# Optimization experiments

Hardware: AMD Instinct MI355X
Metric: run time of the kernel (lower is better)

The kernel has to match this reference:

```python
import jax, jax.numpy as jnp
import numpy as np

NEG_INF = -1e9


def setup_inputs() -> dict:
    key = jax.random.key(0)
    k1, k2, k3 = jax.random.split(key, 3)
    B, S, D, N, K = 8, 4096, 1024, 128, 8
    hidden_states = jax.random.normal(k1, (B, S, D), dtype=jnp.float32)
    sentence_indicator = jnp.sort(
        jax.random.randint(k2, (B, S), 0, N), axis=-1).astype(jnp.int64)
    cls_w = jax.random.normal(k3, (D,), dtype=jnp.float32) * (1.0 / np.sqrt(D))
    cls_b = jnp.zeros((), dtype=jnp.float32)
    return {
        "hidden_states": hidden_states,
        "sentence_indicator": sentence_indicator,
        "cls_w": cls_w,
        "cls_b": cls_b,
        "num_sentences": N,
        "extraction_k": K,
    }


def _selection_loop(hidden_states, sentence_indicator, cls_w, cls_b,
                    num_sentences, extraction_k):
    # --- sentence segment-sum pooling (replaces per-sentence masked-sum loop) ---
    seg_sum = jax.vmap(
        lambda h, ind: jax.ops.segment_sum(h, ind, num_segments=num_sentences)
    )(hidden_states, sentence_indicator)               # [B, N, D]
    counts = jax.vmap(
        lambda ind: jax.ops.segment_sum(
            jnp.ones(ind.shape, jnp.float32), ind, num_segments=num_sentences)
    )(sentence_indicator)                              # [B, N]
    sentence_lens = jnp.clip(counts, 1.0)[..., None]   # [B, N, 1], clamp(min=1)
    sentence_mask0 = (counts > 0).astype(jnp.float32)  # valid-sentence mask [B, N]

    B, N, D = seg_sum.shape

    def step(carry, _):
        cur_sum, cur_len, smask, sel = carry
        combined = cur_sum[:, None, :] + seg_sum           # [B, N, D]
        combined_len = cur_len[:, None, :] + sentence_lens  # [B, N, 1]
        pooled = combined / combined_len                    # [B, N, D]
        logits = jnp.einsum('bnd,d->bn', pooled, cls_w) + cls_b
        logits = jnp.where(smask > 0, logits, NEG_INF)      # mask_tensor
        idx = jnp.argmax(logits, axis=-1)                   # eval path (argmax)
        one_hot = jax.nn.one_hot(idx, N, dtype=jnp.float32)  # [B, N]
        smask = (1.0 - one_hot) * smask
        new_sum = jnp.einsum('bn,bnd->bd', one_hot, combined)
        new_len = jnp.sum(one_hot[..., None] * combined_len, axis=1)  # [B, 1]
        return (new_sum, new_len, smask, sel + one_hot), logits

    init = (jnp.zeros((B, D), jnp.float32),
            jnp.zeros((B, 1), jnp.float32),
            sentence_mask0,
            jnp.zeros((B, N), jnp.float32))
    (_, _, _, selected), all_logits = jax.lax.scan(
        step, init, None, length=extraction_k)
    selected = jnp.clip(selected, 0.0, 1.0)  # clamp(max=1)
    return selected, all_logits  # [B,N], [K,B,N]


def reference(hidden_states, sentence_indicator, cls_w, cls_b,
              num_sentences, extraction_k):
    selected_one_hot, all_logits = _selection_loop(
        hidden_states, sentence_indicator, cls_w, cls_b,
        num_sentences, extraction_k)
    # convert_attention_mask: token is kept iff its sentence was selected
    new_attention_mask = jnp.take_along_axis(
        selected_one_hot, sentence_indicator, axis=1)      # [B, S] float 0/1
    masked_hidden_states = new_attention_mask[..., None] * hidden_states
    return selected_one_hot, all_logits, new_attention_mask, masked_hidden_states
```

## Files before the change

kernel.cpp:

```cpp
#include <hip/hip_runtime.h>

#define B_ 8
#define S_ 4096
#define D_ 1024
#define N_ 128
#define K_ 8
#define NEG_INF_ (-1e9f)

__global__ void tok_dot_kernel(const float* __restrict__ h,
                               const float* __restrict__ cls_w,
                               float* __restrict__ tok_dot) {
    const int lane = threadIdx.x & 63;
    const int gw = (blockIdx.x << 2) + (threadIdx.x >> 6);
    const int t0 = gw << 2;
    const int dofs = lane * 4;

    const float4 w0 = *reinterpret_cast<const float4*>(cls_w + 0 * 256 + dofs);
    const float4 w1 = *reinterpret_cast<const float4*>(cls_w + 1 * 256 + dofs);
    const float4 w2 = *reinterpret_cast<const float4*>(cls_w + 2 * 256 + dofs);
    const float4 w3 = *reinterpret_cast<const float4*>(cls_w + 3 * 256 + dofs);

    float acc[4];
    #pragma unroll
    for (int t = 0; t < 4; ++t) {
        const float* p = h + (size_t)(t0 + t) * D_;
        const float4 v0 = *reinterpret_cast<const float4*>(p + 0 * 256 + dofs);
        const float4 v1 = *reinterpret_cast<const float4*>(p + 1 * 256 + dofs);
        const float4 v2 = *reinterpret_cast<const float4*>(p + 2 * 256 + dofs);
        const float4 v3 = *reinterpret_cast<const float4*>(p + 3 * 256 + dofs);
        acc[t] = v0.x * w0.x + v0.y * w0.y + v0.z * w0.z + v0.w * w0.w
               + v1.x * w1.x + v1.y * w1.y + v1.z * w1.z + v1.w * w1.w
               + v2.x * w2.x + v2.y * w2.y + v2.z * w2.z + v2.w * w2.w
               + v3.x * w3.x + v3.y * w3.y + v3.z * w3.z + v3.w * w3.w;
    }
    for (int off = 32; off > 0; off >>= 1) {
        #pragma unroll
        for (int t = 0; t < 4; ++t) acc[t] += __shfl_down(acc[t], off, 64);
    }
    if (lane == 0) {
        *reinterpret_cast<float4*>(tok_dot + t0) =
            make_float4(acc[0], acc[1], acc[2], acc[3]);
    }
}

__global__ void select_kernel(const float* __restrict__ tok_dot,
                              const int* __restrict__ ind,
                              const float* __restrict__ cls_b,
                              float* __restrict__ out_selected,
                              float* __restrict__ out_logits,
                              float* __restrict__ out_mask) {
    const int b = blockIdx.x;
    const int tid = threadIdx.x;

    __shared__ float td[S_];
    __shared__ int   si[S_];
    __shared__ float sh_part[256];
    __shared__ int   sh_s0[N_], sh_s1[N_];
    __shared__ float sh_dseg[N_], sh_len[N_], sh_msk[N_], sh_sel[N_];

    for (int s = tid; s < S_; s += 256) {
        td[s] = tok_dot[b * S_ + s];
        si[s] = ind[b * S_ + s];
    }
    __syncthreads();

    {
        const int n = tid & (N_ - 1);
        int lo = 0, hi = S_;
        while (lo < hi) { int mid = (lo + hi) >> 1; if (si[mid] < n) lo = mid + 1; else hi = mid; }
        const int s0 = lo;
        lo = s0; hi = S_;
        while (lo < hi) { int mid = (lo + hi) >> 1; if (si[mid] < n + 1) lo = mid + 1; else hi = mid; }
        const int s1 = lo;
        const int mid = (s0 + s1) >> 1;
        const int a = (tid < N_) ? s0 : mid;
        const int e = (tid < N_) ? mid : s1;
        float acc = 0.f;
        for (int s = a; s < e; ++s) acc += td[s];
        sh_part[tid] = acc;
        if (tid < N_) { sh_s0[tid] = s0; sh_s1[tid] = s1; }
    }
    __syncthreads();
    if (tid < N_) {
        const int s0 = sh_s0[tid], s1 = sh_s1[tid];
        sh_dseg[tid] = sh_part[tid] + sh_part[tid + N_];
        sh_len[tid]  = fmaxf((float)(s1 - s0), 1.0f);
        sh_msk[tid]  = (s1 > s0) ? 1.f : 0.f;
    }
    __syncthreads();

    if (tid < 64) {
        const float bias = cls_b[0];
        const float d0 = sh_dseg[tid],      d1 = sh_dseg[tid + 64];
        const float l0 = sh_len[tid],       l1 = sh_len[tid + 64];
        float m0 = sh_msk[tid],             m1 = sh_msk[tid + 64];
        float sel0 = 0.f, sel1 = 0.f;
        float dot = 0.f, len = 0.f;

        for (int k = 0; k < K_; ++k) {
            const float lg0 = (m0 > 0.f) ? (dot + d0) / (len + l0) + bias : NEG_INF_;
            const float lg1 = (m1 > 0.f) ? (dot + d1) / (len + l1) + bias : NEG_INF_;
            out_logits[(size_t)k * (B_ * N_) + b * N_ + tid]      = lg0;
            out_logits[(size_t)k * (B_ * N_) + b * N_ + tid + 64] = lg1;
            float bv; int bi;
            if (lg0 >= lg1) { bv = lg0; bi = tid; } else { bv = lg1; bi = tid + 64; }
            for (int off = 32; off > 0; off >>= 1) {
                const float ov = __shfl_xor(bv, off, 64);
                const int   oi = __shfl_xor(bi, off, 64);
                if (ov > bv || (ov == bv && oi < bi)) { bv = ov; bi = oi; }
            }
            const float dsrc = (bi < 64) ? d0 : d1;
            const float lsrc = (bi < 64) ? l0 : l1;
            dot += __shfl(dsrc, bi & 63, 64);
            len += __shfl(lsrc, bi & 63, 64);
            if ((bi & 63) == tid) {
                if (bi < 64) { m0 = 0.f; sel0 = 1.f; }
                else         { m1 = 0.f; sel1 = 1.f; }
            }
        }
        out_selected[b * N_ + tid]      = sel0;
        out_selected[b * N_ + tid + 64] = sel1;
        sh_sel[tid]      = sel0;
        sh_sel[tid + 64] = sel1;
    }
    __syncthreads();
    for (int s = tid; s < S_; s += 256) {
        out_mask[b * S_ + s] = sh_sel[si[s]];
    }
}

#define TPB_ 16
__global__ void write_kernel(const float* __restrict__ h,
                             const float* __restrict__ out_mask,
                             float* __restrict__ out_masked) {
    const int t0 = blockIdx.x * TPB_;
    const int tid = threadIdx.x;
    float m[TPB_];
    #pragma unroll
    for (int i = 0; i < TPB_; ++i) m[i] = out_mask[t0 + i];
    const float4 z = make_float4(0.f, 0.f, 0.f, 0.f);
    #pragma unroll
    for (int i = 0; i < TPB_; ++i) {
        if (m[i] == 0.f) {
            const size_t base = (size_t)(t0 + i) * D_ + tid * 4;
            *reinterpret_cast<float4*>(out_masked + base) = z;
        }
    }
    #pragma unroll
    for (int i = 0; i < TPB_; ++i) {
        if (m[i] != 0.f) {
            const size_t base = (size_t)(t0 + i) * D_ + tid * 4;
            *reinterpret_cast<float4*>(out_masked + base) =
                *reinterpret_cast<const float4*>(h + base);
        }
    }
}

extern "C" void kernel_launch(void* const* d_in, const int* in_sizes, int n_in,
                              void* d_out, int out_size, void* d_ws, size_t ws_size,
                              hipStream_t stream) {
    const float* h     = (const float*)d_in[0];
    const int*   ind   = (const int*)d_in[1];
    const float* cls_w = (const float*)d_in[2];
    const float* cls_b = (const float*)d_in[3];

    float* out = (float*)d_out;
    float* out_selected = out;
    float* out_logits   = out + 1024;
    float* out_mask     = out + 1024 + 8192;
    float* out_masked   = out + 1024 + 8192 + 32768;

    float* tok_dot = (float*)d_ws;

    tok_dot_kernel<<<dim3(2048), dim3(256), 0, stream>>>(h, cls_w, tok_dot);
    select_kernel<<<dim3(B_), dim3(256), 0, stream>>>(tok_dot, ind, cls_b,
                                                      out_selected, out_logits,
                                                      out_mask);
    write_kernel<<<dim3(B_ * S_ / TPB_), dim3(256), 0, stream>>>(h, out_mask, out_masked);
}
```

Measured before the change: 64.74 us.

## Fuse token-dot and selection kernels with last-block-done atomic counters

```diff
diff --git a/kernel.cpp b/kernel.cpp
--- a/kernel.cpp
+++ b/kernel.cpp
@@ -7,125 +7,140 @@
 #define K_ 8
 #define NEG_INF_ (-1e9f)
 
-__global__ void tok_dot_kernel(const float* __restrict__ h,
-                               const float* __restrict__ cls_w,
-                               float* __restrict__ tok_dot) {
-    const int lane = threadIdx.x & 63;
-    const int gw = (blockIdx.x << 2) + (threadIdx.x >> 6);
-    const int t0 = gw << 2;
+__global__ __launch_bounds__(256, 8)
+void tok_dot_select_kernel(const float* __restrict__ h,
+                           const float* __restrict__ cls_w,
+                           const int* __restrict__ ind,
+                           const float* __restrict__ cls_b,
+                           float* __restrict__ tok_dot,
+                           int* __restrict__ counters,
+                           float* __restrict__ out_selected,
+                           float* __restrict__ out_logits,
+                           float* __restrict__ out_mask) {
+    const int tid = threadIdx.x;
+    const int lane = tid & 63;
+    const int gw = (blockIdx.x << 2) + (tid >> 6);
     const int dofs = lane * 4;
 
-    const float4 w0 = *reinterpret_cast<const float4*>(cls_w + 0 * 256 + dofs);
-    const float4 w1 = *reinterpret_cast<const float4*>(cls_w + 1 * 256 + dofs);
-    const float4 w2 = *reinterpret_cast<const float4*>(cls_w + 2 * 256 + dofs);
-    const float4 w3 = *reinterpret_cast<const float4*>(cls_w + 3 * 256 + dofs);
+    {
+        const float4 w0 = *reinterpret_cast<const float4*>(cls_w + 0 * 256 + dofs);
+        const float4 w1 = *reinterpret_cast<const float4*>(cls_w + 1 * 256 + dofs);
+        const float4 w2 = *reinterpret_cast<const float4*>(cls_w + 2 * 256 + dofs);
+        const float4 w3 = *reinterpret_cast<const float4*>(cls_w + 3 * 256 + dofs);
 
-    float acc[4];
-    #pragma unroll
-    for (int t = 0; t < 4; ++t) {
-        const float* p = h + (size_t)(t0 + t) * D_;
-        const float4 v0 = *reinterpret_cast<const float4*>(p + 0 * 256 + dofs);
-        const float4 v1 = *reinterpret_cast<const float4*>(p + 1 * 256 + dofs);
-        const float4 v2 = *reinterpret_cast<const float4*>(p + 2 * 256 + dofs);
-        const float4 v3 = *reinterpret_cast<const float4*>(p + 3 * 256 + dofs);
-        acc[t] = v0.x * w0.x + v0.y * w0.y + v0.z * w0.z + v0.w * w0.w
-               + v1.x * w1.x + v1.y * w1.y + v1.z * w1.z + v1.w * w1.w
-               + v2.x * w2.x + v2.y * w2.y + v2.z * w2.z + v2.w * w2.w
-               + v3.x * w3.x + v3.y * w3.y + v3.z * w3.z + v3.w * w3.w;
+        float acc[4];
+        #pragma unroll
+        for (int t = 0; t < 4; ++t) {
+            const float* p = h + (size_t)(gw + t * 8192) * D_;
+            const float4 v0 = *reinterpret_cast<const float4*>(p + 0 * 256 + dofs);
+            const float4 v1 = *reinterpret_cast<const float4*>(p + 1 * 256 + dofs);
+            const float4 v2 = *reinterpret_cast<const float4*>(p + 2 * 256 + dofs);
+            const float4 v3 = *reinterpret_cast<const float4*>(p + 3 * 256 + dofs);
+            acc[t] = v0.x * w0.x + v0.y * w0.y + v0.z * w0.z + v0.w * w0.w
+                   + v1.x * w1.x + v1.y * w1.y + v1.z * w1.z + v1.w * w1.w
+                   + v2.x * w2.x + v2.y * w2.y + v2.z * w2.z + v2.w * w2.w
+                   + v3.x * w3.x + v3.y * w3.y + v3.z * w3.z + v3.w * w3.w;
+        }
+        for (int off = 32; off > 0; off >>= 1) {
+            #pragma unroll
+            for (int t = 0; t < 4; ++t) acc[t] += __shfl_down(acc[t], off, 64);
+        }
+        if (lane == 0) {
+            #pragma unroll
+            for (int t = 0; t < 4; ++t) tok_dot[gw + t * 8192] = acc[t];
+        }
     }
-    for (int off = 32; off > 0; off >>= 1) {
-        #pragma unroll
-        for (int t = 0; t < 4; ++t) acc[t] += __shfl_down(acc[t], off, 64);
-    }
-    if (lane == 0) {
-        *reinterpret_cast<float4*>(tok_dot + t0) =
-            make_float4(acc[0], acc[1], acc[2], acc[3]);
-    }
-}
 
-__global__ void select_kernel(const float* __restrict__ tok_dot,
-                              const int* __restrict__ ind,
-                              const float* __restrict__ cls_b,
-                              float* __restrict__ out_selected,
-                              float* __restrict__ out_logits,
-                              float* __restrict__ out_mask) {
-    const int b = blockIdx.x;
-    const int tid = threadIdx.x;
-
-    __shared__ float td[S_];
-    __shared__ int   si[S_];
+    __shared__ int do_batch[4];
     __shared__ float sh_part[256];
     __shared__ int   sh_s0[N_], sh_s1[N_];
     __shared__ float sh_dseg[N_], sh_len[N_], sh_msk[N_], sh_sel[N_];
 
-    for (int s = tid; s < S_; s += 256) {
-        td[s] = tok_dot[b * S_ + s];
-        si[s] = ind[b * S_ + s];
+    __syncthreads();
+    if (tid == 0) {
+        __threadfence();
+        const int c = (blockIdx.x >= 1024) ? 1 : 0;
+        #pragma unroll
+        for (int j = 0; j < 4; ++j) {
+            const int b = c + 2 * j;
+            const int t = atomicAdd(&counters[b], 1);
+            do_batch[j] = (t == 1023) ? b : -1;
+        }
     }
     __syncthreads();
 
-    {
-        const int n = tid & (N_ - 1);
-        int lo = 0, hi = S_;
-        while (lo < hi) { int mid = (lo + hi) >> 1; if (si[mid] < n) lo = mid + 1; else hi = mid; }
-        const int s0 = lo;
-        lo = s0; hi = S_;
-        while (lo < hi) { int mid = (lo + hi) >> 1; if (si[mid] < n + 1) lo = mid + 1; else hi = mid; }
-        const int s1 = lo;
-        const int mid = (s0 + s1) >> 1;
-        const int a = (tid < N_) ? s0 : mid;
-        const int e = (tid < N_) ? mid : s1;
-        float acc = 0.f;
-        for (int s = a; s < e; ++s) acc += td[s];
-        sh_part[tid] = acc;
-        if (tid < N_) { sh_s0[tid] = s0; sh_s1[tid] = s1; }
-    }
-    __syncthreads();
-    if (tid < N_) {
-        const int s0 = sh_s0[tid], s1 = sh_s1[tid];
-        sh_dseg[tid] = sh_part[tid] + sh_part[tid + N_];
-        sh_len[tid]  = fmaxf((float)(s1 - s0), 1.0f);
-        sh_msk[tid]  = (s1 > s0) ? 1.f : 0.f;
-    }
-    __syncthreads();
+    for (int j = 0; j < 4; ++j) {
+        const int b = do_batch[j];
+        if (b < 0) continue;
+        __threadfence();
 
-    if (tid < 64) {
-        const float bias = cls_b[0];
-        const float d0 = sh_dseg[tid],      d1 = sh_dseg[tid + 64];
-        const float l0 = sh_len[tid],       l1 = sh_len[tid + 64];
-        float m0 = sh_msk[tid],             m1 = sh_msk[tid + 64];
-        float sel0 = 0.f, sel1 = 0.f;
-        float dot = 0.f, len = 0.f;
+        const int*   sib = ind + b * S_;
+        const float* tdb = tok_dot + b * S_;
 
-        for (int k = 0; k < K_; ++k) {
-            const float lg0 = (m0 > 0.f) ? (dot + d0) / (len + l0) + bias : NEG_INF_;
-            const float lg1 = (m1 > 0.f) ? (dot + d1) / (len + l1) + bias : NEG_INF_;
-            out_logits[(size_t)k * (B_ * N_) + b * N_ + tid]      = lg0;
-            out_logits[(size_t)k * (B_ * N_) + b * N_ + tid + 64] = lg1;
-            float bv; int bi;
-            if (lg0 >= lg1) { bv = lg0; bi = tid; } else { bv = lg1; bi = tid + 64; }
-            for (int off = 32; off > 0; off >>= 1) {
-                const float ov = __shfl_xor(bv, off, 64);
-                const int   oi = __shfl_xor(bi, off, 64);
-                if (ov > bv || (ov == bv && oi < bi)) { bv = ov; bi = oi; }
+        {
+            const int n = tid & (N_ - 1);
+            int lo = 0, hi = S_;
+            while (lo < hi) { int mid = (lo + hi) >> 1; if (sib[mid] < n) lo = mid + 1; else hi = mid; }
+            const int s0 = lo;
+            lo = s0; hi = S_;
+            while (lo < hi) { int mid = (lo + hi) >> 1; if (sib[mid] < n + 1) lo = mid + 1; else hi = mid; }
+            const int s1 = lo;
+            const int mid = (s0 + s1) >> 1;
+            const int a = (tid < N_) ? s0 : mid;
+            const int e = (tid < N_) ? mid : s1;
+            float acc = 0.f;
+            for (int s = a; s < e; ++s) acc += tdb[s];
+            sh_part[tid] = acc;
+            if (tid < N_) { sh_s0[tid] = s0; sh_s1[tid] = s1; }
+        }
+        __syncthreads();
+        if (tid < N_) {
+            const int s0 = sh_s0[tid], s1 = sh_s1[tid];
+            sh_dseg[tid] = sh_part[tid] + sh_part[tid + N_];
+            sh_len[tid]  = fmaxf((float)(s1 - s0), 1.0f);
+            sh_msk[tid]  = (s1 > s0) ? 1.f : 0.f;
+        }
+        __syncthreads();
+
+        if (tid < 64) {
+            const float bias = cls_b[0];
+            const float d0 = sh_dseg[tid],      d1 = sh_dseg[tid + 64];
+            const float l0 = sh_len[tid],       l1 = sh_len[tid + 64];
+            float m0 = sh_msk[tid],             m1 = sh_msk[tid + 64];
+            float sel0 = 0.f, sel1 = 0.f;
+            float dot = 0.f, len = 0.f;
+
+            for (int k = 0; k < K_; ++k) {
+                const float lg0 = (m0 > 0.f) ? (dot + d0) / (len + l0) + bias : NEG_INF_;
+                const float lg1 = (m1 > 0.f) ? (dot + d1) / (len + l1) + bias : NEG_INF_;
+                out_logits[(size_t)k * (B_ * N_) + b * N_ + tid]      = lg0;
+                out_logits[(size_t)k * (B_ * N_) + b * N_ + tid + 64] = lg1;
+                float bv; int bi;
+                if (lg0 >= lg1) { bv = lg0; bi = tid; } else { bv = lg1; bi = tid + 64; }
+                for (int off = 32; off > 0; off >>= 1) {
+                    const float ov = __shfl_xor(bv, off, 64);
+                    const int   oi = __shfl_xor(bi, off, 64);
+                    if (ov > bv || (ov == bv && oi < bi)) { bv = ov; bi = oi; }
+                }
+                const float dsrc = (bi < 64) ? d0 : d1;
+                const float lsrc = (bi < 64) ? l0 : l1;
+                dot += __shfl(dsrc, bi & 63, 64);
+                len += __shfl(lsrc, bi & 63, 64);
+                if ((bi & 63) == tid) {
+                    if (bi < 64) { m0 = 0.f; sel0 = 1.f; }
+                    else         { m1 = 0.f; sel1 = 1.f; }
+                }
             }
-            const float dsrc = (bi < 64) ? d0 : d1;
-            const float lsrc = (bi < 64) ? l0 : l1;
-            dot += __shfl(dsrc, bi & 63, 64);
-            len += __shfl(lsrc, bi & 63, 64);
-            if ((bi & 63) == tid) {
-                if (bi < 64) { m0 = 0.f; sel0 = 1.f; }
-                else         { m1 = 0.f; sel1 = 1.f; }
-            }
+            out_selected[b * N_ + tid]      = sel0;
+            out_selected[b * N_ + tid + 64] = sel1;
+            sh_sel[tid]      = sel0;
+            sh_sel[tid + 64] = sel1;
         }
-        out_selected[b * N_ + tid]      = sel0;
-        out_selected[b * N_ + tid + 64] = sel1;
-        sh_sel[tid]      = sel0;
-        sh_sel[tid + 64] = sel1;
-    }
-    __syncthreads();
-    for (int s = tid; s < S_; s += 256) {
-        out_mask[b * S_ + s] = sh_sel[si[s]];
+        __syncthreads();
+        for (int s = tid; s < S_; s += 256) {
+            out_mask[b * S_ + s] = sh_sel[sib[s]];
+        }
+        __syncthreads();
     }
 }
 
@@ -170,11 +185,13 @@
     float* out_mask     = out + 1024 + 8192;
     float* out_masked   = out + 1024 + 8192 + 32768;
 
-    float* tok_dot = (float*)d_ws;
+    char* ws = (char*)d_ws;
+    float* tok_dot  = (float*)ws;
+    int*   counters = (int*)(ws + (size_t)B_ * S_ * 4);
 
-    tok_dot_kernel<<<dim3(2048), dim3(256), 0, stream>>>(h, cls_w, tok_dot);
-    select_kernel<<<dim3(B_), dim3(256), 0, stream>>>(tok_dot, ind, cls_b,
-                                                      out_selected, out_logits,
-                                                      out_mask);
+    hipMemsetAsync(counters, 0, 8 * sizeof(int), stream);
+    tok_dot_select_kernel<<<dim3(2048), dim3(256), 0, stream>>>(
+        h, cls_w, ind, cls_b, tok_dot, counters,
+        out_selected, out_logits, out_mask);
     write_kernel<<<dim3(B_ * S_ / TPB_), dim3(256), 0, stream>>>(h, out_mask, out_masked);
 }
```

Result: slower. 217.7 us (+236.3%).
